# Optimization experiments

Measured on AMD Instinct MI355X. Metric: run time of the kernel, lower is better.

Reference implementation:

```python
import jax, jax.numpy as jnp
import numpy as np

# ---- polar grid config (matches init_kwargs) ----
N_RADIAL = 48
N_ANGULAR = 72
RADIAL_EDGES = jnp.arange(2.0, 51.0, dtype=jnp.float32)            # 49 edges, [2, 50] m
ANGLE_EDGES = jnp.linspace(-np.pi, np.pi, N_ANGULAR + 1).astype(jnp.float32)
Z_MIN, Z_MAX = -3.0, 5.0
MAX_PTS = 64      # max_points_per_voxel
MAX_VOX = 3000    # max_voxels (< H = 3456, truncation path active)
H = N_RADIAL * N_ANGULAR


def setup_inputs() -> dict:
    key = jax.random.key(0)
    pts = jax.random.normal(key, (4_000_000, 5), dtype=jnp.float32)
    # scale xy to ~[-45,45] m and z to ~[-6,6] m so masks keep a realistic fraction
    scale = jnp.array([15.0, 15.0, 2.0, 1.0, 1.0], dtype=jnp.float32)
    return {"points": pts * scale}


def reference(points):
    N, C = points.shape
    x, y, z = points[:, 0], points[:, 1], points[:, 2]
    r = jnp.sqrt(x * x + y * y)
    theta = jnp.arctan2(y, x)

    valid = ((z >= Z_MIN) & (z < Z_MAX)
             & (r >= RADIAL_EDGES[0]) & (r < RADIAL_EDGES[-1])
             & (theta >= ANGLE_EDGES[0]) & (theta < ANGLE_EDGES[-1]))

    # torch.searchsorted(right=False) == jnp side='left'
    r_idx = jnp.clip(jnp.searchsorted(RADIAL_EDGES, r, side='left') - 1, 0, N_RADIAL - 1)
    t_idx = jnp.clip(jnp.searchsorted(ANGLE_EDGES, theta, side='left') - 1, 0, N_ANGULAR - 1)

    # invalid points get sentinel hash H (out of range -> dropped by scatter)
    vhash = jnp.where(valid, r_idx * N_ANGULAR + t_idx, H).astype(jnp.int32)

    # sort points by voxel hash (stable, matching torch.argsort semantics here)
    order = jnp.argsort(vhash)
    sh = vhash[order]                       # [N] sorted hashes
    sp = points[order]                      # [N, C] points in hash order

    # rank of each point within its voxel = position - first occurrence of its hash
    first = jnp.searchsorted(sh, sh, side='left')
    rank = jnp.arange(N, dtype=jnp.int32) - first.astype(jnp.int32)

    # dense hard-voxelization scatter: keep first MAX_PTS points per voxel.
    # out-of-range (sh==H or rank>=MAX_PTS) indices are dropped.
    vox_dense = jnp.zeros((H, MAX_PTS, C), dtype=points.dtype).at[sh, rank].set(sp, mode='drop')

    counts = jax.ops.segment_sum(jnp.ones_like(vhash), vhash, num_segments=H + 1)[:H]
    npts_dense = jnp.minimum(counts, MAX_PTS).astype(jnp.int32)

    # unique occupied hashes in ascending order -> output slots (first MAX_VOX kept)
    occupied = counts > 0
    slot = jnp.cumsum(occupied.astype(jnp.int32)) - 1
    slot = jnp.where(occupied & (slot < MAX_VOX), slot, MAX_VOX)  # MAX_VOX => dropped
    slot2hash = jnp.zeros((MAX_VOX,), jnp.int32).at[slot].set(jnp.arange(H, dtype=jnp.int32), mode='drop')
    slot_valid = jnp.zeros((MAX_VOX,), bool).at[slot].set(True, mode='drop')

    voxels = jnp.where(slot_valid[:, None, None], vox_dense[slot2hash], 0.0)  # [MAX_VOX, MAX_PTS, C]
    num_points = jnp.where(slot_valid, npts_dense[slot2hash], 0)

    ri = slot2hash // N_ANGULAR
    ti = slot2hash % N_ANGULAR
    coords = jnp.where(slot_valid[:, None],
                       jnp.stack([ri, ti, jnp.zeros_like(ri)], axis=1), 0).astype(jnp.int32)

    r_c = 0.5 * (RADIAL_EDGES[ri] + RADIAL_EDGES[ri + 1])
    t_c = 0.5 * (ANGLE_EDGES[ti] + ANGLE_EDGES[ti + 1])
    centers = jnp.where(slot_valid[:, None],
                        jnp.stack([r_c * jnp.cos(t_c), r_c * jnp.sin(t_c)], axis=1), 0.0)

    return voxels, coords, num_points, centers
```

## Files before the change

kernel.cpp:

```cpp
#include <hip/hip_runtime.h>
#include <math.h>

#define NRAD 48
#define NANG 72
#define HV   3456
#define HVW  864
#define MAXP 64
#define MAXV 3000
#define BLK  256
#define CHT  64
#define TILE 4096
#define SUBT 1024
#define NCH  16

#define OFF_C   (MAXV*MAXP*5)
#define OFF_N   (OFF_C + MAXV*3)
#define OFF_X   (OFF_N + MAXV)

#define PI_F 3.14159265358979323846f

__device__ __forceinline__ float angle_edge(int j) {
  const double PI = 3.14159265358979311599796346854;
  const double step = (PI - (-PI)) / 72.0;
  if (j == 72) return (float)PI;
  return (float)(-PI + (double)j * step);
}

__global__ __launch_bounds__(BLK) void k_hist(
    const float* __restrict__ pts, int N, int tile, int n4, int tailN,
    unsigned char* __restrict__ hist, unsigned short* __restrict__ bins,
    float4* __restrict__ out4) {
  __shared__ int lh[HV];
  __shared__ float eang[73];
  int t = blockIdx.x, tid = threadIdx.x;
  for (int j = t * BLK + tid; j < n4; j += gridDim.x * BLK)
    out4[j] = make_float4(0.f, 0.f, 0.f, 0.f);
  if (t == 0 && tid < tailN) ((float*)out4)[(size_t)n4 * 4 + tid] = 0.f;
  for (int i = tid; i < HV; i += BLK) lh[i] = 0;
  if (tid < 73) eang[tid] = angle_edge(tid);
  __syncthreads();
  int base = t * tile;
  int end  = min(base + tile, N);
  for (int i = base + tid; i < end; i += BLK) {
    size_t p = (size_t)i * 5;
    float x = pts[p], y = pts[p + 1], z = pts[p + 2];
    float r = __fsqrt_rn(__fadd_rn(__fmul_rn(x, x), __fmul_rn(y, y)));
    int b = HV;
    if (z >= -3.0f && z < 5.0f && r >= 2.0f && r < 50.0f) {
      int ri = (int)ceilf(r) - 3;
      ri = max(0, min(NRAD - 1, ri));
      float ax = fabsf(x), ay = fabsf(y);
      float u = fminf(ax, ay), U = fmaxf(ax, ay);
      bool big = u > 0.41421356f * U;
      float num = big ? (U - u) : u;
      float den = big ? (U + u) : U;
      float v = num / den;
      float s = v * v;
      float a = 0.05882353f;
      a = a * s - 0.06666667f;
      a = a * s + 0.07692308f;
      a = a * s - 0.09090909f;
      a = a * s + 0.11111111f;
      a = a * s - 0.14285714f;
      a = a * s + 0.2f;
      a = a * s - 0.33333333f;
      a = a * s + 1.0f;
      float pp = v * a;
      float th1 = big ? (0.78539816f - pp) : pp;
      if (ay > ax) th1 = 1.57079633f - th1;
      if (x < 0.0f) th1 = PI_F - th1;
      float that = copysignf(th1, y);
      int g = (int)floorf((that + PI_F) * 11.459155902616465f);
      g = max(0, min(NANG - 1, g));
      while (g > 0 && !(eang[g] < that)) g--;
      while (g < NANG - 1 && eang[g + 1] < that) g++;
      float d0 = that - eang[g];
      float d1 = eang[g + 1] - that;
      const float GUARD = 2e-5f;
      if (d0 > GUARD && d1 > GUARD) {
        b = ri * NANG + g;
      } else {
        float th = (float)atan2((double)y, (double)x);
        if (th >= eang[0] && th < eang[72]) {
          int gg = g;
          while (gg > 0 && !(eang[gg] < th)) gg--;
          while (gg < NANG - 1 && eang[gg + 1] < th) gg++;
          b = ri * NANG + max(0, min(NANG - 1, gg));
        } else {
          b = HV;
        }
      }
    }
    bins[i] = (unsigned short)b;
    if (b < HV) atomicAdd(&lh[b], 1);
  }
  __syncthreads();
  unsigned char* ht = hist + (size_t)t * HV;
  for (int i = tid; i < HV; i += BLK) ht[i] = (unsigned char)min(lh[i], 64);
}

__global__ void k_scan_a(const unsigned int* __restrict__ hist32, int NT,
                         unsigned int* __restrict__ part32) {
  int w = blockIdx.x * BLK + threadIdx.x;
  int c = blockIdx.y;
  if (w >= HVW) return;
  int t0 = c * CHT, t1 = min(t0 + CHT, NT);
  int s0 = 0, s1 = 0, s2 = 0, s3 = 0;
  for (int t = t0; t < t1; ++t) {
    unsigned int v = hist32[(size_t)t * HVW + w];
    s0 = min(s0 + (int)(v & 255u), 64);
    s1 = min(s1 + (int)((v >> 8) & 255u), 64);
    s2 = min(s2 + (int)((v >> 16) & 255u), 64);
    s3 = min(s3 + (int)(v >> 24), 64);
  }
  part32[(size_t)c * HVW + w] = (unsigned)s0 | ((unsigned)s1 << 8) |
                                ((unsigned)s2 << 16) | ((unsigned)s3 << 24);
}

__global__ __launch_bounds__(1024) void k_bsc(unsigned int* __restrict__ part32, int NC,
                                              int* __restrict__ soh,
                                              float* __restrict__ out) {
  __shared__ float eang[73];
  __shared__ int ssum[1024];
  int tid = threadIdx.x;
  if (tid < 73) eang[tid] = angle_edge(tid);
  int c0 = 0, c1 = 0, c2 = 0, c3 = 0;
  if (tid < HVW) {
    int r0 = 0, r1 = 0, r2 = 0, r3 = 0;
    for (int c = 0; c < NC; ++c) {
      size_t o = (size_t)c * HVW + tid;
      unsigned int v = part32[o];
      part32[o] = (unsigned)r0 | ((unsigned)r1 << 8) |
                  ((unsigned)r2 << 16) | ((unsigned)r3 << 24);
      r0 = min(r0 + (int)(v & 255u), 64);
      r1 = min(r1 + (int)((v >> 8) & 255u), 64);
      r2 = min(r2 + (int)((v >> 16) & 255u), 64);
      r3 = min(r3 + (int)(v >> 24), 64);
    }
    c0 = r0; c1 = r1; c2 = r2; c3 = r3;
  }
  int occ = (c0 > 0) + (c1 > 0) + (c2 > 0) + (c3 > 0);
  ssum[tid] = occ;
  __syncthreads();
  for (int off = 1; off < 1024; off <<= 1) {
    int v = (tid >= off) ? ssum[tid - off] : 0;
    __syncthreads();
    ssum[tid] += v;
    __syncthreads();
  }
  int base = ssum[tid] - occ;
  if (tid < HVW) {
    int cs[4] = {c0, c1, c2, c3};
#pragma unroll
    for (int k = 0; k < 4; ++k) {
      int h = tid * 4 + k;
      int cnt = cs[k];
      int s = -1;
      if (cnt > 0) {
        if (base < MAXV) s = base;
        base++;
      }
      soh[h] = s;
      if (s >= 0) {
        int ri = h / NANG, ti = h % NANG;
        out[OFF_C + s * 3 + 0] = (float)ri;
        out[OFF_C + s * 3 + 1] = (float)ti;
        out[OFF_C + s * 3 + 2] = 0.0f;
        out[OFF_N + s] = (float)cnt;
        float rc = 2.5f + (float)ri;
        float tc = 0.5f * (eang[ti] + eang[ti + 1]);
        out[OFF_X + s * 2 + 0] = rc * cosf(tc);
        out[OFF_X + s * 2 + 1] = rc * sinf(tc);
      }
    }
  }
}

__global__ void k_scan_c(unsigned int* __restrict__ hist32, int NT,
                         const unsigned int* __restrict__ part32) {
  int w = blockIdx.x * BLK + threadIdx.x;
  int c = blockIdx.y;
  if (w >= HVW) return;
  int t0 = c * CHT, t1 = min(t0 + CHT, NT);
  unsigned int pv = part32[(size_t)c * HVW + w];
  int r0 = pv & 255u, r1 = (pv >> 8) & 255u, r2 = (pv >> 16) & 255u, r3 = pv >> 24;
  for (int t = t0; t < t1; ++t) {
    size_t o = (size_t)t * HVW + w;
    unsigned int v = hist32[o];
    hist32[o] = (unsigned)r0 | ((unsigned)r1 << 8) |
                ((unsigned)r2 << 16) | ((unsigned)r3 << 24);
    r0 = min(r0 + (int)(v & 255u), 64);
    r1 = min(r1 + (int)((v >> 8) & 255u), 64);
    r2 = min(r2 + (int)((v >> 16) & 255u), 64);
    r3 = min(r3 + (int)(v >> 24), 64);
  }
}

__global__ __launch_bounds__(BLK) void k_scatter_fast(
    const float* __restrict__ pts, int N,
    const unsigned char* __restrict__ hist, const unsigned short* __restrict__ bins,
    const int* __restrict__ soh, float* __restrict__ out) {
  __shared__ unsigned int whd[4 * HV / 2];
  unsigned short (*wh)[HV] = (unsigned short (*)[HV])whd;
  int t = blockIdx.x;
  int tid = threadIdx.x;
  int lane = tid & 63, wv = tid >> 6;
  for (int i = tid; i < 4 * HV / 2; i += BLK) whd[i] = 0u;
  __syncthreads();
  int base = t * TILE;
  int end  = min(base + TILE, N);
  int sb = base + wv * SUBT;
  int se = min(sb + SUBT, end);
  unsigned short lb[NCH], lr[NCH];
  const unsigned long long lmask = (1ULL << lane) - 1ULL;
#pragma unroll
  for (int c = 0; c < NCH; ++c) {
    int i = sb + c * 64 + lane;
    int b = 4095;
    if (i < se) { int bi = bins[i]; if (bi < HV) b = bi; }
    unsigned long long m = ~0ULL;
#pragma unroll
    for (int k = 0; k < 12; ++k) {
      unsigned long long bal = __ballot((b >> k) & 1);
      m &= ((b >> k) & 1) ? bal : ~bal;
    }
    int rho = __popcll(m & lmask);
    int kap = __popcll(m);
    int cv = 0;
    if (b != 4095) {
      cv = wh[wv][b];
      if (rho == 0) wh[wv][b] = (unsigned short)(cv + kap);
    }
    lb[c] = (unsigned short)b;
    lr[c] = (unsigned short)(cv + rho);
  }
  __syncthreads();
  for (int j = tid; j < HV; j += BLK) {
    int a0 = wh[0][j], a1 = wh[1][j], a2 = wh[2][j];
    wh[0][j] = 0;
    wh[1][j] = (unsigned short)a0;
    wh[2][j] = (unsigned short)(a0 + a1);
    wh[3][j] = (unsigned short)(a0 + a1 + a2);
  }
  __syncthreads();
  const unsigned char* ht = hist + (size_t)t * HV;
#pragma unroll
  for (int c = 0; c < NCH; ++c) {
    int b = lb[c];
    if (b == 4095) continue;
    int rank = (int)ht[b] + (int)wh[wv][b] + (int)lr[c];
    if (rank < MAXP) {
      int s = soh[b];
      if (s >= 0) {
        int i = sb + c * 64 + lane;
        size_t dst = (size_t)(s * MAXP + rank) * 5;
        size_t src = (size_t)i * 5;
        out[dst + 0] = pts[src + 0];
        out[dst + 1] = pts[src + 1];
        out[dst + 2] = pts[src + 2];
        out[dst + 3] = pts[src + 3];
        out[dst + 4] = pts[src + 4];
      }
    }
  }
}

__global__ void k_scatter_gen(const float* __restrict__ pts, int N, int tile,
                              const unsigned char* __restrict__ hist,
                              const unsigned short* __restrict__ bins,
                              const int* __restrict__ soh,
                              float* __restrict__ out) {
  __shared__ int cur[HV + 1];
  int t = blockIdx.x;
  int tid = threadIdx.x;
  const unsigned char* ht = hist + (size_t)t * HV;
  for (int i = tid; i < HV + 1; i += BLK) cur[i] = (i < HV) ? (int)ht[i] : 0;
  __syncthreads();
  int base = t * tile;
  int end  = min(base + tile, N);
  int lane = tid & 63, wv = tid >> 6;
  for (int g = base; g < base + tile; g += BLK) {
    int i = g + tid;
    bool act = (i < end);
    int b = act ? (int)bins[i] : 0x10000;
    int rho = 0, kap = 0;
    for (int j = 0; j < 64; ++j) {
      int bj = __shfl(b, j, 64);
      if (bj == b) { kap++; if (j < lane) rho++; }
    }
    int rank = 0x7FFFFFFF;
    for (int w = 0; w < 4; ++w) {
      if (wv == w && act) {
        int bs = cur[b];
        rank = bs + rho;
        if (rho == 0) cur[b] = bs + kap;
      }
      __syncthreads();
    }
    if (act && rank < MAXP && b < HV) {
      int s = soh[b];
      if (s >= 0) {
        size_t dst = (size_t)(s * MAXP + rank) * 5;
        size_t src = (size_t)i * 5;
        out[dst + 0] = pts[src + 0];
        out[dst + 1] = pts[src + 1];
        out[dst + 2] = pts[src + 2];
        out[dst + 3] = pts[src + 3];
        out[dst + 4] = pts[src + 4];
      }
    }
  }
}

extern "C" void kernel_launch(void* const* d_in, const int* in_sizes, int n_in,
                              void* d_out, int out_size, void* d_ws, size_t ws_size,
                              hipStream_t stream) {
  const float* pts = (const float*)d_in[0];
  int N = in_sizes[0] / 5;
  float* out = (float*)d_out;

  auto align = [](size_t x) { return (x + 255) & ~(size_t)255; };
  int tile = TILE, NT = 1, NC = 1;
  size_t o_hist = 0, o_part = 0, o_soh = 0, o_bins = 0;
  for (;;) {
    NT = (N + tile - 1) / tile;
    NC = (NT + CHT - 1) / CHT;
    o_hist = 0;
    o_part = align(o_hist + (size_t)NT * HV);
    o_soh  = align(o_part + (size_t)NC * HV);
    o_bins = align(o_soh + (size_t)HV * 4);
    size_t need = o_bins + (size_t)N * 2;
    if (need <= ws_size || tile >= (1 << 22)) break;
    tile <<= 1;
  }

  char* w = (char*)d_ws;
  unsigned char* hist = (unsigned char*)(w + o_hist);
  unsigned int*  hist32 = (unsigned int*)hist;
  unsigned int*  part32 = (unsigned int*)(w + o_part);
  int* soh = (int*)(w + o_soh);
  unsigned short* bins = (unsigned short*)(w + o_bins);

  int n4 = out_size / 4;
  int tailN = out_size - n4 * 4;

  k_hist<<<NT, BLK, 0, stream>>>(pts, N, tile, n4, tailN, hist, bins, (float4*)out);
  dim3 ga((HVW + BLK - 1) / BLK, NC);
  k_scan_a<<<ga, BLK, 0, stream>>>(hist32, NT, part32);
  k_bsc<<<1, 1024, 0, stream>>>(part32, NC, soh, out);
  k_scan_c<<<ga, BLK, 0, stream>>>(hist32, NT, part32);
  if (tile == TILE) {
    k_scatter_fast<<<NT, BLK, 0, stream>>>(pts, N, hist, bins, soh, out);
  } else {
    k_scatter_gen<<<NT, BLK, 0, stream>>>(pts, N, tile, hist, bins, soh, out);
  }
}
```

Baseline: 93.05 us.

## Vectorize histogram point loads, batch scan loads, skip saturated bins in scatter

The histogram kernel now handles four points per thread, reading them as five float4 loads and writing their bins as one ushort4, with the binning logic moved into a shared helper. The block scan loads 16 partial rows into registers before doing the serial prefix, so the loads can overlap. The fast scatter drops points whose bin is already full (prefix count of 64) before the ballot-based ranking, and skips a whole chunk when no lane remains. The aim is fewer memory transactions and less ranking work, at the cost of more registers per thread and a scalar tail loop for leftover points.

```diff
diff --git a/kernel.cpp b/kernel.cpp
--- a/kernel.cpp
+++ b/kernel.cpp
@@ -24,6 +24,49 @@
   const double step = (PI - (-PI)) / 72.0;
   if (j == 72) return (float)PI;
   return (float)(-PI + (double)j * step);
+}
+
+__device__ __forceinline__ int point_bin(float x, float y, float z,
+                                         const float* __restrict__ eang) {
+  float r = __fsqrt_rn(__fadd_rn(__fmul_rn(x, x), __fmul_rn(y, y)));
+  if (!(z >= -3.0f && z < 5.0f && r >= 2.0f && r < 50.0f)) return HV;
+  int ri = (int)ceilf(r) - 3;
+  ri = max(0, min(NRAD - 1, ri));
+  float ax = fabsf(x), ay = fabsf(y);
+  float u = fminf(ax, ay), U = fmaxf(ax, ay);
+  bool big = u > 0.41421356f * U;
+  float num = big ? (U - u) : u;
+  float den = big ? (U + u) : U;
+  float v = num / den;
+  float s = v * v;
+  float a = 0.05882353f;
+  a = a * s - 0.06666667f;
+  a = a * s + 0.07692308f;
+  a = a * s - 0.09090909f;
+  a = a * s + 0.11111111f;
+  a = a * s - 0.14285714f;
+  a = a * s + 0.2f;
+  a = a * s - 0.33333333f;
+  a = a * s + 1.0f;
+  float pp = v * a;
+  float th1 = big ? (0.78539816f - pp) : pp;
+  if (ay > ax) th1 = 1.57079633f - th1;
+  if (x < 0.0f) th1 = PI_F - th1;
+  float that = copysignf(th1, y);
+  int g = (int)floorf((that + PI_F) * 11.459155902616465f);
+  g = max(0, min(NANG - 1, g));
+  while (g > 0 && !(eang[g] < that)) g--;
+  while (g < NANG - 1 && eang[g + 1] < that) g++;
+  float d0 = that - eang[g];
+  float d1 = eang[g + 1] - that;
+  const float GUARD = 2e-5f;
+  if (d0 > GUARD && d1 > GUARD) return ri * NANG + g;
+  float th = (float)atan2((double)y, (double)x);
+  if (!(th >= eang[0] && th < eang[72])) return HV;
+  int gg = g;
+  while (gg > 0 && !(eang[gg] < th)) gg--;
+  while (gg < NANG - 1 && eang[gg + 1] < th) gg++;
+  return ri * NANG + max(0, min(NANG - 1, gg));
 }
 
 __global__ __launch_bounds__(BLK) void k_hist(
@@ -41,56 +84,25 @@
   __syncthreads();
   int base = t * tile;
   int end  = min(base + tile, N);
-  for (int i = base + tid; i < end; i += BLK) {
+  int endq = base + (((end - base) >> 2) << 2);
+  const float4* p4 = (const float4*)pts;
+  for (int i0 = base + (tid << 2); i0 < endq; i0 += (BLK << 2)) {
+    size_t q = (size_t)(i0 >> 2) * 5;
+    float4 v0 = p4[q], v1 = p4[q + 1], v2 = p4[q + 2], v3 = p4[q + 3], v4 = p4[q + 4];
+    int b0 = point_bin(v0.x, v0.y, v0.z, eang);
+    int b1 = point_bin(v1.y, v1.z, v1.w, eang);
+    int b2 = point_bin(v2.z, v2.w, v3.x, eang);
+    int b3 = point_bin(v3.w, v4.x, v4.y, eang);
+    *(ushort4*)(bins + i0) = make_ushort4((unsigned short)b0, (unsigned short)b1,
+                                          (unsigned short)b2, (unsigned short)b3);
+    if (b0 < HV) atomicAdd(&lh[b0], 1);
+    if (b1 < HV) atomicAdd(&lh[b1], 1);
+    if (b2 < HV) atomicAdd(&lh[b2], 1);
+    if (b3 < HV) atomicAdd(&lh[b3], 1);
+  }
+  for (int i = endq + tid; i < end; i += BLK) {
     size_t p = (size_t)i * 5;
-    float x = pts[p], y = pts[p + 1], z = pts[p + 2];
-    float r = __fsqrt_rn(__fadd_rn(__fmul_rn(x, x), __fmul_rn(y, y)));
-    int b = HV;
-    if (z >= -3.0f && z < 5.0f && r >= 2.0f && r < 50.0f) {
-      int ri = (int)ceilf(r) - 3;
-      ri = max(0, min(NRAD - 1, ri));
-      float ax = fabsf(x), ay = fabsf(y);
-      float u = fminf(ax, ay), U = fmaxf(ax, ay);
-      bool big = u > 0.41421356f * U;
-      float num = big ? (U - u) : u;
-      float den = big ? (U + u) : U;
-      float v = num / den;
-      float s = v * v;
-      float a = 0.05882353f;
-      a = a * s - 0.06666667f;
-      a = a * s + 0.07692308f;
-      a = a * s - 0.09090909f;
-      a = a * s + 0.11111111f;
-      a = a * s - 0.14285714f;
-      a = a * s + 0.2f;
-      a = a * s - 0.33333333f;
-      a = a * s + 1.0f;
-      float pp = v * a;
-      float th1 = big ? (0.78539816f - pp) : pp;
-      if (ay > ax) th1 = 1.57079633f - th1;
-      if (x < 0.0f) th1 = PI_F - th1;
-      float that = copysignf(th1, y);
-      int g = (int)floorf((that + PI_F) * 11.459155902616465f);
-      g = max(0, min(NANG - 1, g));
-      while (g > 0 && !(eang[g] < that)) g--;
-      while (g < NANG - 1 && eang[g + 1] < that) g++;
-      float d0 = that - eang[g];
-      float d1 = eang[g + 1] - that;
-      const float GUARD = 2e-5f;
-      if (d0 > GUARD && d1 > GUARD) {
-        b = ri * NANG + g;
-      } else {
-        float th = (float)atan2((double)y, (double)x);
-        if (th >= eang[0] && th < eang[72]) {
-          int gg = g;
-          while (gg > 0 && !(eang[gg] < th)) gg--;
-          while (gg < NANG - 1 && eang[gg + 1] < th) gg++;
-          b = ri * NANG + max(0, min(NANG - 1, gg));
-        } else {
-          b = HV;
-        }
-      }
-    }
+    int b = point_bin(pts[p], pts[p + 1], pts[p + 2], eang);
     bins[i] = (unsigned short)b;
     if (b < HV) atomicAdd(&lh[b], 1);
   }
@@ -124,22 +136,29 @@
   __shared__ int ssum[1024];
   int tid = threadIdx.x;
   if (tid < 73) eang[tid] = angle_edge(tid);
-  int c0 = 0, c1 = 0, c2 = 0, c3 = 0;
-  if (tid < HVW) {
-    int r0 = 0, r1 = 0, r2 = 0, r3 = 0;
-    for (int c = 0; c < NC; ++c) {
-      size_t o = (size_t)c * HVW + tid;
-      unsigned int v = part32[o];
-      part32[o] = (unsigned)r0 | ((unsigned)r1 << 8) |
-                  ((unsigned)r2 << 16) | ((unsigned)r3 << 24);
-      r0 = min(r0 + (int)(v & 255u), 64);
-      r1 = min(r1 + (int)((v >> 8) & 255u), 64);
-      r2 = min(r2 + (int)((v >> 16) & 255u), 64);
-      r3 = min(r3 + (int)(v >> 24), 64);
-    }
-    c0 = r0; c1 = r1; c2 = r2; c3 = r3;
-  }
+  int r0 = 0, r1 = 0, r2 = 0, r3 = 0;
+  for (int cb = 0; cb < NC; cb += 16) {
+    unsigned int vv[16];
+#pragma unroll
+    for (int k = 0; k < 16; ++k) {
+      int c = cb + k;
+      vv[k] = (tid < HVW && c < NC) ? part32[(size_t)c * HVW + tid] : 0u;
+    }
+#pragma unroll
+    for (int k = 0; k < 16; ++k) {
+      int c = cb + k;
+      if (tid < HVW && c < NC)
+        part32[(size_t)c * HVW + tid] = (unsigned)r0 | ((unsigned)r1 << 8) |
+                                        ((unsigned)r2 << 16) | ((unsigned)r3 << 24);
+      r0 = min(r0 + (int)(vv[k] & 255u), 64);
+      r1 = min(r1 + (int)((vv[k] >> 8) & 255u), 64);
+      r2 = min(r2 + (int)((vv[k] >> 16) & 255u), 64);
+      r3 = min(r3 + (int)(vv[k] >> 24), 64);
+    }
+  }
+  int c0 = r0, c1 = r1, c2 = r2, c3 = r3;
   int occ = (c0 > 0) + (c1 > 0) + (c2 > 0) + (c3 > 0);
+  if (tid >= HVW) occ = 0;
   ssum[tid] = occ;
   __syncthreads();
   for (int off = 1; off < 1024; off <<= 1) {
@@ -211,13 +230,20 @@
   int end  = min(base + TILE, N);
   int sb = base + wv * SUBT;
   int se = min(sb + SUBT, end);
+  const unsigned char* ht = hist + (size_t)t * HV;
   unsigned short lb[NCH], lr[NCH];
   const unsigned long long lmask = (1ULL << lane) - 1ULL;
 #pragma unroll
   for (int c = 0; c < NCH; ++c) {
     int i = sb + c * 64 + lane;
     int b = 4095;
-    if (i < se) { int bi = bins[i]; if (bi < HV) b = bi; }
+    if (i < se) {
+      int bi = bins[i];
+      if (bi < HV && ht[bi] < 64) b = bi;
+    }
+    lb[c] = (unsigned short)b;
+    lr[c] = 0;
+    if (__ballot(b != 4095) == 0ULL) continue;
     unsigned long long m = ~0ULL;
 #pragma unroll
     for (int k = 0; k < 12; ++k) {
@@ -231,7 +257,6 @@
       cv = wh[wv][b];
       if (rho == 0) wh[wv][b] = (unsigned short)(cv + kap);
     }
-    lb[c] = (unsigned short)b;
     lr[c] = (unsigned short)(cv + rho);
   }
   __syncthreads();
@@ -243,7 +268,6 @@
     wh[3][j] = (unsigned short)(a0 + a1 + a2);
   }
   __syncthreads();
-  const unsigned char* ht = hist + (size_t)t * HV;
 #pragma unroll
   for (int c = 0; c < NCH; ++c) {
     int b = lb[c];
```

New measurement: 92.00 us. About the same (-1.1%).
